# Optimization experiments

Hardware: AMD Instinct MI355X
Metric: run time of the kernel (lower is better)

## Reference

```python
import jax, jax.numpy as jnp
import numpy as np

D_PARAM = 20   # module's d
S1 = 1         # module's s1
D_WIN = D_PARAM + S1   # 21: sliding-window size -> 441 displacement channels
PAD = D_PARAM // 2     # 10


def setup_inputs() -> dict:
    key = jax.random.key(0)
    k1, k2 = jax.random.split(key)
    B, C, W, H = 4, 128, 128, 128
    x1 = jax.random.normal(k1, (B, C, W, H), dtype=jnp.float32)
    x2 = jax.random.normal(k2, (B, C, W, H), dtype=jnp.float32)
    return {"x1": x1, "x2": x2}


def _correlation(x1, x2):
    # out[b, di*D+dj, i, j] = sum_c x1_padded[b, c, i+di, j+dj] * x2[b, c, i, j]
    # This reproduces: pad x1 by PAD, unfold 21x21 windows stride 1, and for each
    # pixel take the dot product over channels with x2[b,:,i,j] (the 1x1 conv2d
    # in the original triple loop). Flatten order of torch is (di, dj) row-major.
    b, c, w, h = x1.shape
    x1p = jnp.pad(x1, ((0, 0), (0, 0), (PAD, PAD), (PAD, PAD)))  # [b,c,w+20,h+20]
    rows_out = []
    for di in range(D_WIN):  # small fixed displacement loop (21 iters)
        rows = jax.lax.slice_in_dim(x1p, di, di + w, axis=2)  # [b,c,w,h+20]
        # stack 21 horizontal shifts -> [b,c,w,h,D_WIN]
        win = jnp.stack(
            [jax.lax.slice_in_dim(rows, dj, dj + h, axis=3) for dj in range(D_WIN)],
            axis=-1,
        )
        # contract over channels: [b, D_WIN(dj), w, h]
        rows_out.append(jnp.einsum('bcwhd,bcwh->bdwh', win, x2))
    out = jnp.stack(rows_out, axis=1)  # [b, D_WIN(di), D_WIN(dj), w, h]
    return out.reshape(b, D_WIN * D_WIN, w, h)


def reference(x1, x2):
    return _correlation(x1, x2)
```

## Files before the change

### kernel.cpp

```cpp
#include <hip/hip_runtime.h>


#define NB 4
#define NC 128
#define NW 128
#define NH 128
#define DW 21
#define PAD 10
#define NROW_T 148
#define NCOL_T 160
#define NCH 441
#define PS 37
#define SCOLS 52
#define SUS (SCOLS * NC)
#define ROW_US (NCOL_T * NC)

typedef __attribute__((ext_vector_type(8))) short short8;
typedef __attribute__((ext_vector_type(4))) float float4v;

__device__ inline ushort f2bf(float f) {
    union { float f; uint u; } v; v.f = f;
    const uint u = v.u;
    return (ushort)((u + 0x7fffu + ((u >> 16) & 1u)) >> 16);
}

__device__ inline void async_copy16(const void* g, void* l) {
    __builtin_amdgcn_global_load_lds(
        (const __attribute__((address_space(1))) void*)g,
        (__attribute__((address_space(3))) void*)l, 16, 0, 0);
}

__device__ inline void stage_row(const ushort* src, ushort* dst, int t) {
    const char* s = (const char*)src;
    char* d = (char*)dst;
    #pragma unroll
    for (int it = 0; it < 3; ++it) {
        const int off = it * 4096 + t * 16;
        async_copy16(s + off, d + off);
    }
    if (t < 64) {
        const int off = 12288 + t * 16;
        async_copy16(s + off, d + off);
    }
}

__global__ __launch_bounds__(256) void transpose_x1(const float* __restrict__ x1,
                                                    ushort* __restrict__ x1T) {
    __shared__ uint tile[128][65];
    const int t = threadIdx.x;
    const int b = blockIdx.x / NROW_T;
    const int r = blockIdx.x % NROW_T;
    const int w = r - PAD;
    const bool inr = (w >= 0 && w < NW);
    if (inr) {
        #pragma unroll
        for (int it = 0; it < 8; ++it) {
            const int u = it * 256 + t;
            const int g4 = u & 31;
            const int cp = u >> 5;
            const float4 va = *(const float4*)&x1[(((size_t)b * NC + 2 * cp    ) * NW + w) * NH + g4 * 4];
            const float4 vb = *(const float4*)&x1[(((size_t)b * NC + 2 * cp + 1) * NW + w) * NH + g4 * 4];
            tile[g4 * 4 + 0][cp] = (uint)f2bf(va.x) | ((uint)f2bf(vb.x) << 16);
            tile[g4 * 4 + 1][cp] = (uint)f2bf(va.y) | ((uint)f2bf(vb.y) << 16);
            tile[g4 * 4 + 2][cp] = (uint)f2bf(va.z) | ((uint)f2bf(vb.z) << 16);
            tile[g4 * 4 + 3][cp] = (uint)f2bf(va.w) | ((uint)f2bf(vb.w) << 16);
        }
    }
    __syncthreads();
    #pragma unroll
    for (int it = 0; it < 10; ++it) {
        const int u = it * 256 + t;
        const int cg = u & 15;
        const int col = u >> 4;
        uint4 v = make_uint4(0, 0, 0, 0);
        const int h = col - PAD;
        if (inr && h >= 0 && h < NH) {
            v.x = tile[h][cg * 4 + 0];
            v.y = tile[h][cg * 4 + 1];
            v.z = tile[h][cg * 4 + 2];
            v.w = tile[h][cg * 4 + 3];
        }
        const int chunk = cg ^ (col & 15);
        *(uint4*)&x1T[(((size_t)b * NROW_T + r) * NCOL_T + col) * NC + chunk * 8] = v;
    }
}

__global__ __launch_bounds__(256) void corr_mfma(const ushort* __restrict__ x1T,
                                                 const float* __restrict__ x2,
                                                 float* __restrict__ out) {
    __shared__ ushort win[4][SUS];
    __shared__ float patch[4][16 * PS];

    const int t = threadIdx.x;
    const int wave = t >> 6;
    const int lane = t & 63;
    const int n16 = lane & 15;
    const int q = lane >> 4;

    const int b = blockIdx.x >> 7;
    const int rem = blockIdx.x & 127;
    const int jq = rem & 3;
    const int iq = rem >> 2;
    const int i0 = iq * 4;
    const int col0 = jq * 32;
    const int i = i0 + wave;

    const ushort* xbase = x1T + (size_t)(b * NROW_T) * ROW_US + (size_t)col0 * NC;

    #pragma unroll
    for (int r = 0; r < 4; ++r)
        stage_row(xbase + (size_t)(i0 + r) * ROW_US, win[r], t);

    short8 Bf[2][4];
    #pragma unroll
    for (int nt = 0; nt < 2; ++nt) {
        const int jc = col0 + nt * 16 + n16;
        #pragma unroll
        for (int k4 = 0; k4 < 4; ++k4) {
            short8 s;
            #pragma unroll
            for (int e = 0; e < 8; ++e) {
                const int c = k4 * 32 + q * 8 + e;
                s[e] = (short)f2bf(x2[(((size_t)b * NC + c) * NW + i) * NH + jc]);
            }
            Bf[nt][k4] = s;
        }
    }

    __syncthreads();

    float* P = &patch[wave][0];

    for (int di = 0; di < DW; ++di) {
        const ushort* A = win[(di + wave) & 3];

        float4v a00 = {0.f,0.f,0.f,0.f}, a01 = {0.f,0.f,0.f,0.f}, a02 = {0.f,0.f,0.f,0.f};
        float4v a10 = {0.f,0.f,0.f,0.f}, a11 = {0.f,0.f,0.f,0.f}, a12 = {0.f,0.f,0.f,0.f};
        #pragma unroll
        for (int k4 = 0; k4 < 4; ++k4) {
            const int kc = q + 4 * k4;
            const int c0 = (0  + n16);
            const int c1 = (16 + n16);
            const int c2 = (32 + n16);
            const int c3 = (36 + n16);
            const short8 A0 = *(const short8*)&A[c0 * NC + ((kc ^ (c0 & 15)) & 15) * 8];
            const short8 A1 = *(const short8*)&A[c1 * NC + ((kc ^ (c1 & 15)) & 15) * 8];
            const short8 A2 = *(const short8*)&A[c2 * NC + ((kc ^ (c2 & 15)) & 15) * 8];
            const short8 A3 = *(const short8*)&A[c3 * NC + ((kc ^ (c3 & 15)) & 15) * 8];
            a00 = __builtin_amdgcn_mfma_f32_16x16x32_bf16(A0, Bf[0][k4], a00, 0, 0, 0);
            a01 = __builtin_amdgcn_mfma_f32_16x16x32_bf16(A1, Bf[0][k4], a01, 0, 0, 0);
            a02 = __builtin_amdgcn_mfma_f32_16x16x32_bf16(A2, Bf[0][k4], a02, 0, 0, 0);
            a10 = __builtin_amdgcn_mfma_f32_16x16x32_bf16(A1, Bf[1][k4], a10, 0, 0, 0);
            a11 = __builtin_amdgcn_mfma_f32_16x16x32_bf16(A2, Bf[1][k4], a11, 0, 0, 0);
            a12 = __builtin_amdgcn_mfma_f32_16x16x32_bf16(A3, Bf[1][k4], a12, 0, 0, 0);
        }

        __syncthreads();
        if (di < DW - 1)
            stage_row(xbase + (size_t)(i0 + di + 4) * ROW_US, win[di & 3], t);

        #pragma unroll
        for (int nt = 0; nt < 2; ++nt) {
            const float4v va = nt ? a10 : a00;
            const float4v vb = nt ? a11 : a01;
            const float4v vc = nt ? a12 : a02;
            #pragma unroll
            for (int reg = 0; reg < 4; ++reg) {
                P[n16 * PS + q * 4 + reg]      = va[reg];
                P[n16 * PS + 16 + q * 4 + reg] = vb[reg];
            }
            if (q == (nt ? 3 : 0)) {
                #pragma unroll
                for (int reg = 0; reg < 4; ++reg)
                    P[n16 * PS + 32 + reg] = vc[reg];
            }
            #pragma unroll
            for (int it2 = 0; it2 < 2; ++it2) {
                const int u = it2 * 64 + lane;
                if (u < 84) {
                    const int dj = u >> 2;
                    const int jj = (u & 3) * 4;
                    float4v v;
                    #pragma unroll
                    for (int p = 0; p < 4; ++p)
                        v[p] = P[(jj + p) * (PS + 1) + dj];
                    *(float4v*)&out[(((size_t)(b * NCH + di * DW + dj)) * NW + i) * NH
                                    + col0 + nt * 16 + jj] = v;
                }
            }
        }

        __syncthreads();
    }
}

extern "C" void kernel_launch(void* const* d_in, const int* in_sizes, int n_in,
                              void* d_out, int out_size, void* d_ws, size_t ws_size,
                              hipStream_t stream) {
    const float* x1 = (const float*)d_in[0];
    const float* x2 = (const float*)d_in[1];
    float* out = (float*)d_out;
    ushort* x1T = (ushort*)d_ws;
    transpose_x1<<<dim3(NB * NROW_T), dim3(256), 0, stream>>>(x1, x1T);
    corr_mfma<<<dim3(NB * 32 * 4), dim3(256), 0, stream>>>(x1T, x2, out);
}
```

Before: 194.4 us.

## Use five-slot row ring and remap blocks for batch interleaving

Grows the LDS window ring from 4 to 5 row buffers so the prefetch of the next x1T row can be issued right after the current fragments are loaded into registers, without the mid-loop barrier. All A fragments are now preloaded into registers before the MFMA chain. Block indices are also remapped so consecutive blocks cycle across batches and image halves, changing L2/HBM access locality. The change adds LDS and register pressure, which may reduce occupancy.

```diff
diff --git a/kernel.cpp b/kernel.cpp
--- a/kernel.cpp
+++ b/kernel.cpp
@@ -88,7 +88,7 @@
 __global__ __launch_bounds__(256) void corr_mfma(const ushort* __restrict__ x1T,
                                                  const float* __restrict__ x2,
                                                  float* __restrict__ out) {
-    __shared__ ushort win[4][SUS];
+    __shared__ ushort win[5][SUS];
     __shared__ float patch[4][16 * PS];
 
     const int t = threadIdx.x;
@@ -97,10 +97,12 @@
     const int n16 = lane & 15;
     const int q = lane >> 4;
 
-    const int b = blockIdx.x >> 7;
-    const int rem = blockIdx.x & 127;
-    const int jq = rem & 3;
-    const int iq = rem >> 2;
+    const int n = blockIdx.x;
+    const int b = (n & 7) >> 1;
+    const int ihalf = n & 1;
+    const int slot = n >> 3;
+    const int iq = ihalf * 16 + (slot >> 2);
+    const int jq = slot & 3;
     const int i0 = iq * 4;
     const int col0 = jq * 32;
     const int i = i0 + wave;
@@ -132,32 +134,34 @@
     float* P = &patch[wave][0];
 
     for (int di = 0; di < DW; ++di) {
-        const ushort* A = win[(di + wave) & 3];
+        const ushort* A = win[(di + wave) % 5];
+
+        short8 Af[4][4];
+        #pragma unroll
+        for (int k4 = 0; k4 < 4; ++k4) {
+            const int kc = q + 4 * k4;
+            #pragma unroll
+            for (int tl = 0; tl < 4; ++tl) {
+                const int base = (tl < 3) ? tl * 16 : 36;
+                const int c = base + n16;
+                Af[tl][k4] = *(const short8*)&A[c * NC + ((kc ^ (c & 15)) & 15) * 8];
+            }
+        }
+
+        if (di < DW - 1)
+            stage_row(xbase + (size_t)(i0 + di + 4) * ROW_US, win[(di + 4) % 5], t);
 
         float4v a00 = {0.f,0.f,0.f,0.f}, a01 = {0.f,0.f,0.f,0.f}, a02 = {0.f,0.f,0.f,0.f};
         float4v a10 = {0.f,0.f,0.f,0.f}, a11 = {0.f,0.f,0.f,0.f}, a12 = {0.f,0.f,0.f,0.f};
         #pragma unroll
         for (int k4 = 0; k4 < 4; ++k4) {
-            const int kc = q + 4 * k4;
-            const int c0 = (0  + n16);
-            const int c1 = (16 + n16);
-            const int c2 = (32 + n16);
-            const int c3 = (36 + n16);
-            const short8 A0 = *(const short8*)&A[c0 * NC + ((kc ^ (c0 & 15)) & 15) * 8];
-            const short8 A1 = *(const short8*)&A[c1 * NC + ((kc ^ (c1 & 15)) & 15) * 8];
-            const short8 A2 = *(const short8*)&A[c2 * NC + ((kc ^ (c2 & 15)) & 15) * 8];
-            const short8 A3 = *(const short8*)&A[c3 * NC + ((kc ^ (c3 & 15)) & 15) * 8];
-            a00 = __builtin_amdgcn_mfma_f32_16x16x32_bf16(A0, Bf[0][k4], a00, 0, 0, 0);
-            a01 = __builtin_amdgcn_mfma_f32_16x16x32_bf16(A1, Bf[0][k4], a01, 0, 0, 0);
-            a02 = __builtin_amdgcn_mfma_f32_16x16x32_bf16(A2, Bf[0][k4], a02, 0, 0, 0);
-            a10 = __builtin_amdgcn_mfma_f32_16x16x32_bf16(A1, Bf[1][k4], a10, 0, 0, 0);
-            a11 = __builtin_amdgcn_mfma_f32_16x16x32_bf16(A2, Bf[1][k4], a11, 0, 0, 0);
-            a12 = __builtin_amdgcn_mfma_f32_16x16x32_bf16(A3, Bf[1][k4], a12, 0, 0, 0);
-        }
-
-        __syncthreads();
-        if (di < DW - 1)
-            stage_row(xbase + (size_t)(i0 + di + 4) * ROW_US, win[di & 3], t);
+            a00 = __builtin_amdgcn_mfma_f32_16x16x32_bf16(Af[0][k4], Bf[0][k4], a00, 0, 0, 0);
+            a01 = __builtin_amdgcn_mfma_f32_16x16x32_bf16(Af[1][k4], Bf[0][k4], a01, 0, 0, 0);
+            a02 = __builtin_amdgcn_mfma_f32_16x16x32_bf16(Af[2][k4], Bf[0][k4], a02, 0, 0, 0);
+            a10 = __builtin_amdgcn_mfma_f32_16x16x32_bf16(Af[1][k4], Bf[1][k4], a10, 0, 0, 0);
+            a11 = __builtin_amdgcn_mfma_f32_16x16x32_bf16(Af[2][k4], Bf[1][k4], a11, 0, 0, 0);
+            a12 = __builtin_amdgcn_mfma_f32_16x16x32_bf16(Af[3][k4], Bf[1][k4], a12, 0, 0, 0);
+        }
 
         #pragma unroll
         for (int nt = 0; nt < 2; ++nt) {
```

New measurement: 188.1 us. 1.03x faster.
